# Performance work log

Hardware: AMD Instinct MI355X
Metric: run time of the kernel (lower is better)

## Reference

```python
import jax, jax.numpy as jnp
import numpy as np

# dims: S=seq (attention axis 0), B=batch, Din=input_dim, E=adjusted_dim,
# NEXP=num_experts, HID=expert hidden, DOUT=output_dim, NH=heads, TOPK=top_k
S, B, Din, E, NEXP, HID, DOUT, NH, TOPK = 1024, 8, 768, 768, 10, 256, 768, 8, 2
LN_EPS = 1e-5


def setup_inputs() -> dict:
    key = jax.random.key(0)
    ks = jax.random.split(key, 10)
    s = 0.02
    return {
        "x": jax.random.normal(ks[0], (S, B, Din), jnp.float32),
        # input_projection: Linear(Din -> E)
        "Wp": jax.random.normal(ks[1], (E, Din), jnp.float32) * s,
        "bp": jnp.zeros((E,), jnp.float32),
        # MultiheadAttention packed in-proj (3E, E) and out-proj (E, E)
        "Win": jax.random.normal(ks[2], (3 * E, E), jnp.float32) * s,
        "bin_": jnp.zeros((3 * E,), jnp.float32),
        "Wo": jax.random.normal(ks[3], (E, E), jnp.float32) * s,
        "bo": jnp.zeros((E,), jnp.float32),
        # gate: Linear(E -> NEXP)
        "Wg": jax.random.normal(ks[4], (NEXP, E), jnp.float32) * s,
        "bg": jnp.zeros((NEXP,), jnp.float32),
        # experts: NEXP x (Linear(E->HID), ReLU, Linear(HID->DOUT))
        "W1": jax.random.normal(ks[5], (NEXP, E, HID), jnp.float32) * s,
        "b1": jnp.zeros((NEXP, HID), jnp.float32),
        "W2": jax.random.normal(ks[6], (NEXP, HID, DOUT), jnp.float32) * s,
        "b2": jnp.zeros((NEXP, DOUT), jnp.float32),
        # LayerNorm(DOUT)
        "gamma": jnp.ones((DOUT,), jnp.float32),
        "beta": jnp.zeros((DOUT,), jnp.float32),
    }


def reference(x, Wp, bp, Win, bin_, Wo, bo, Wg, bg, W1, b1, W2, b2, gamma, beta):
    hd = E // NH
    # input projection
    h = jnp.einsum('sbd,ed->sbe', x, Wp) + bp  # (S,B,E)
    # self-attention (torch MHA, seq-first, no mask)
    qkv = jnp.einsum('sbe,fe->sbf', h, Win) + bin_  # (S,B,3E)
    q, k, v = jnp.split(qkv, 3, axis=-1)
    q = q.reshape(S, B, NH, hd) * (hd ** -0.5)
    k = k.reshape(S, B, NH, hd)
    v = v.reshape(S, B, NH, hd)
    scores = jnp.einsum('sbhd,tbhd->bhst', q, k)       # (B,NH,S,S)
    attn = jax.nn.softmax(scores, axis=-1)
    ctx = jnp.einsum('bhst,tbhd->sbhd', attn, v).reshape(S, B, E)
    h = jnp.einsum('sbe,fe->sbf', ctx, Wo) + bo        # (S,B,E)
    # top-k gating
    gate_probs = jax.nn.softmax(jnp.einsum('sbe,ne->sbn', h, Wg) + bg, axis=-1)
    top_p, top_i = jax.lax.top_k(gate_probs, TOPK)     # (S,B,TOPK)
    top_p = top_p / jnp.sum(top_p, axis=-1, keepdims=True)
    # combine weights: (S,B,NEXP), zero for unselected experts
    combine = jnp.sum(top_p[..., None] * jax.nn.one_hot(top_i, NEXP, dtype=h.dtype), axis=-2)
    # per-expert MLP, weighted combine (dense dispatch, same math as masked loop)
    eh = jax.nn.relu(jnp.einsum('sbe,neh->sbnh', h, W1) + b1)  # (S,B,NEXP,HID)
    moe = jnp.einsum('sbnh,nho,sbn->sbo', eh, W2, combine) + jnp.einsum('sbn,no->sbo', combine, b2)
    # LayerNorm over DOUT
    mu = jnp.mean(moe, axis=-1, keepdims=True)
    var = jnp.mean((moe - mu) ** 2, axis=-1, keepdims=True)
    moe = (moe - mu) * jax.lax.rsqrt(var + LN_EPS) * gamma + beta
    # attn_weights: head-averaged (B,S,S), then raw .view to (S,B,-1), mean last
    aw = jnp.mean(attn, axis=1)            # (B,S,S)
    aw = aw.reshape(S, B, -1)              # memory reinterpretation as in torch .view
    aw = jnp.mean(aw, axis=-1, keepdims=True)  # (S,B,1)
    return moe * aw, aw
```

## Files before the change

kernel.cpp:

```cpp
#include <hip/hip_runtime.h>
#include <math.h>

#define S_    1024
#define B_    8
#define E_    768
#define NH_   8
#define HD_   96
#define NEXP_ 10
#define HID_  256
#define DOUT_ 768
#define TOK_  (S_*B_)
#define OUT0_ (TOK_*DOUT_)

#define OFF_H1   0
#define OFF_QB   6291456
#define OFF_KB   12582912
#define OFF_VB   18874368
#define OFF_H2   25165824
#define OFF_TW   31457280
#define OFF_INT  (31457280 + 16384)

__device__ __forceinline__ void gload_lds16(const float* g, float* l) {
    __builtin_amdgcn_global_load_lds((const __attribute__((address_space(1))) void*)(g),
                                     (__attribute__((address_space(3))) void*)(l), 16, 0, 0);
}

__global__ void init_counts(int* counts) {
    if (threadIdx.x < 16) counts[threadIdx.x] = 0;
}

template<int MODE>
__global__ __launch_bounds__(256)
void gemm_abt(const float* __restrict__ A, const float* __restrict__ W,
              const float* __restrict__ bias, float* __restrict__ C,
              int M, int N, int K,
              float* __restrict__ qb, float* __restrict__ kb, float* __restrict__ vb)
{
    __shared__ float Ast[16][132];
    __shared__ float Wst[16][132];
    const int tid = threadIdx.x;
    const int tx = tid & 15, ty = tid >> 4;
    const int m0 = blockIdx.x * 128, n0 = blockIdx.y * 128;
    const int lrow = tid >> 2, lkq = tid & 3;

    const float* Ab0 = A + (size_t)(m0 + lrow)*K + lkq*4;
    const float* Ab1 = Ab0 + (size_t)64*K;
    const float* Wb0 = W + (size_t)(n0 + lrow)*K + lkq*4;
    const float* Wb1 = Wb0 + (size_t)64*K;

    float4 pa0 = *(const float4*)Ab0;
    float4 pa1 = *(const float4*)Ab1;
    float4 pw0 = *(const float4*)Wb0;
    float4 pw1 = *(const float4*)Wb1;

    float acc[8][8];
    #pragma unroll
    for (int i = 0; i < 8; i++)
        #pragma unroll
        for (int j = 0; j < 8; j++) acc[i][j] = 0.f;

    for (int k0 = 0;;) {
        Ast[lkq*4+0][lrow]    = pa0.x; Ast[lkq*4+1][lrow]    = pa0.y;
        Ast[lkq*4+2][lrow]    = pa0.z; Ast[lkq*4+3][lrow]    = pa0.w;
        Ast[lkq*4+0][lrow+64] = pa1.x; Ast[lkq*4+1][lrow+64] = pa1.y;
        Ast[lkq*4+2][lrow+64] = pa1.z; Ast[lkq*4+3][lrow+64] = pa1.w;
        Wst[lkq*4+0][lrow]    = pw0.x; Wst[lkq*4+1][lrow]    = pw0.y;
        Wst[lkq*4+2][lrow]    = pw0.z; Wst[lkq*4+3][lrow]    = pw0.w;
        Wst[lkq*4+0][lrow+64] = pw1.x; Wst[lkq*4+1][lrow+64] = pw1.y;
        Wst[lkq*4+2][lrow+64] = pw1.z; Wst[lkq*4+3][lrow+64] = pw1.w;
        __syncthreads();
        k0 += 16;
        const bool more = (k0 < K);
        if (more) {
            pa0 = *(const float4*)(Ab0 + k0);
            pa1 = *(const float4*)(Ab1 + k0);
            pw0 = *(const float4*)(Wb0 + k0);
            pw1 = *(const float4*)(Wb1 + k0);
        }
        #pragma unroll
        for (int kk = 0; kk < 16; kk++) {
            float a[8], w[8];
            *(float4*)&a[0] = *(const float4*)&Ast[kk][ty*4];
            *(float4*)&a[4] = *(const float4*)&Ast[kk][64 + ty*4];
            *(float4*)&w[0] = *(const float4*)&Wst[kk][tx*4];
            *(float4*)&w[4] = *(const float4*)&Wst[kk][64 + tx*4];
            #pragma unroll
            for (int i = 0; i < 8; i++)
                #pragma unroll
                for (int j = 0; j < 8; j++)
                    acc[i][j] = fmaf(a[i], w[j], acc[i][j]);
        }
        __syncthreads();
        if (!more) break;
    }

    const float QS = 0.10206207261596575f;
    #pragma unroll
    for (int i = 0; i < 8; i++) {
        const int m = m0 + ((i < 4) ? (ty*4 + i) : (64 + ty*4 + i - 4));
        #pragma unroll
        for (int jq = 0; jq < 2; jq++) {
            const int nb = n0 + (jq ? (64 + tx*4) : (tx*4));
            const float4 bv = *(const float4*)(bias + nb);
            float4 v;
            v.x = acc[i][jq*4+0] + bv.x;
            v.y = acc[i][jq*4+1] + bv.y;
            v.z = acc[i][jq*4+2] + bv.z;
            v.w = acc[i][jq*4+3] + bv.w;
            if (MODE == 0) {
                *(float4*)(C + (size_t)m*N + nb) = v;
            } else {
                const int s = m >> 3, b = m & 7;
                const int which = nb / E_;
                const int e = nb - which*E_;
                const int h = e / HD_, d = e - h*HD_;
                float* dst = (which == 0) ? qb : (which == 1) ? kb : vb;
                if (which == 0) { v.x *= QS; v.y *= QS; v.z *= QS; v.w *= QS; }
                *(float4*)(dst + ((size_t)((b<<3) + h)*S_ + s)*HD_ + d) = v;
            }
        }
    }
}

__global__ __launch_bounds__(256, 2)
void attn_kernel(const float* __restrict__ qb, const float* __restrict__ kb,
                 const float* __restrict__ vb, float* __restrict__ ctxb)
{
    __shared__ float Ks[64*96];
    __shared__ float Vs[64*96];
    const int tid = threadIdx.x;
    const int wave = tid >> 6;
    const int lane = tid & 63;
    const int part = lane >> 5;
    const int rloc = wave*32 + (lane & 31);
    const int bh = blockIdx.y;
    const int srow = blockIdx.x*128 + rloc;
    const float* qp = qb + ((size_t)bh*S_ + srow)*HD_;
    const float* kbase = kb + (size_t)bh*S_*HD_;
    const float* vbase = vb + (size_t)bh*S_*HD_;

    float q[96], cx[96];
    #pragma unroll
    for (int i = 0; i < 24; i++) *(float4*)&q[i*4] = *(const float4*)(qp + i*4);
    #pragma unroll
    for (int i = 0; i < 96; i++) cx[i] = 0.f;
    float l = 0.f;

    for (int t0 = 0; t0 < S_; t0 += 64) {
        #pragma unroll
        for (int j = 0; j < 6; j++) {
            const int f = j*256 + tid;
            const int r = f / 24, c = f % 24;
            gload_lds16(kbase + (size_t)(t0+r)*HD_ + c*4, &Ks[f*4]);
            gload_lds16(vbase + (size_t)(t0+r)*HD_ + c*4, &Vs[f*4]);
        }
        __syncthreads();
        const int tb = part*32;
        for (int tt2 = 0; tt2 < 32; tt2++) {
            const float* kr = &Ks[(size_t)(tb+tt2)*96];
            float sacc[4] = {0.f, 0.f, 0.f, 0.f};
            #pragma unroll
            for (int i = 0; i < 24; i++) {
                const float4 kv = *(const float4*)(kr + i*4);
                float sv = sacc[i & 3];
                sv = fmaf(q[i*4+0], kv.x, sv); sv = fmaf(q[i*4+1], kv.y, sv);
                sv = fmaf(q[i*4+2], kv.z, sv); sv = fmaf(q[i*4+3], kv.w, sv);
                sacc[i & 3] = sv;
            }
            const float p = __expf((sacc[0]+sacc[1])+(sacc[2]+sacc[3]));
            l += p;
            const float* vr = &Vs[(size_t)(tb+tt2)*96];
            #pragma unroll
            for (int i = 0; i < 24; i++) {
                const float4 vv = *(const float4*)(vr + i*4);
                cx[i*4+0] = fmaf(p, vv.x, cx[i*4+0]);
                cx[i*4+1] = fmaf(p, vv.y, cx[i*4+1]);
                cx[i*4+2] = fmaf(p, vv.z, cx[i*4+2]);
                cx[i*4+3] = fmaf(p, vv.w, cx[i*4+3]);
            }
        }
        __syncthreads();
    }
    l += __shfl_xor(l, 32);
    #pragma unroll
    for (int i = 0; i < 96; i++) cx[i] += __shfl_xor(cx[i], 32);
    if (part == 0) {
        const float inv = 1.f / l;
        const int b = bh >> 3, h = bh & 7;
        float* op = ctxb + ((size_t)srow*B_ + b)*E_ + h*HD_;
        #pragma unroll
        for (int i = 0; i < 24; i++) {
            float4 o;
            o.x = cx[i*4+0]*inv; o.y = cx[i*4+1]*inv;
            o.z = cx[i*4+2]*inv; o.w = cx[i*4+3]*inv;
            *(float4*)(op + i*4) = o;
        }
    }
}

__global__ __launch_bounds__(256)
void gate_kernel(const float* __restrict__ h2, const float* __restrict__ Wg,
                 const float* __restrict__ bg, int* __restrict__ tix,
                 float* __restrict__ tw, int* __restrict__ counts)
{
    const int lane = threadIdx.x & 63;
    const int tok = blockIdx.x*4 + (threadIdx.x >> 6);
    const float* hr = h2 + (size_t)tok*E_;
    float part[NEXP_];
    #pragma unroll
    for (int n = 0; n < NEXP_; n++) part[n] = 0.f;
    for (int i = 0; i < 12; i++) {
        const float xv = hr[i*64 + lane];
        #pragma unroll
        for (int n = 0; n < NEXP_; n++)
            part[n] = fmaf(xv, Wg[n*E_ + i*64 + lane], part[n]);
    }
    #pragma unroll
    for (int n = 0; n < NEXP_; n++) {
        float v = part[n];
        for (int off = 32; off > 0; off >>= 1) v += __shfl_xor(v, off);
        part[n] = v;
    }
    if (lane == 0) {
        float lg[NEXP_];
        #pragma unroll
        for (int n = 0; n < NEXP_; n++) lg[n] = part[n] + bg[n];
        int i1 = 0; float l1 = lg[0];
        #pragma unroll
        for (int n = 1; n < NEXP_; n++) if (lg[n] > l1) { l1 = lg[n]; i1 = n; }
        int i2 = -1; float l2 = -1e30f;
        #pragma unroll
        for (int n = 0; n < NEXP_; n++) if (n != i1 && lg[n] > l2) { l2 = lg[n]; i2 = n; }
        const float p = __expf(l2 - l1);
        const float w1 = 1.f / (1.f + p);
        tix[tok*2]   = i1; tix[tok*2+1] = i2;
        tw[tok*2]    = w1; tw[tok*2+1]  = 1.f - w1;
        atomicAdd(&counts[i1], 1);
        atomicAdd(&counts[i2], 1);
    }
}

__global__ void scan_kernel(const int* __restrict__ counts, int* __restrict__ offsets,
                            int* __restrict__ cursor) {
    if (threadIdx.x == 0) {
        int run = 0;
        for (int e = 0; e < NEXP_; e++) { offsets[e] = run; cursor[e] = run; run += counts[e]; }
    }
}

__global__ __launch_bounds__(256)
void scatter_kernel(const int* __restrict__ tix, int* __restrict__ cursor,
                    int* __restrict__ elist) {
    const int tok = blockIdx.x*256 + threadIdx.x;
    #pragma unroll
    for (int slot = 0; slot < 2; slot++) {
        const int e = tix[tok*2 + slot];
        const int pos = atomicAdd(&cursor[e], 1);
        elist[pos] = tok*2 + slot;
    }
}

__global__ __launch_bounds__(256)
void expert_mlp1(const float* __restrict__ h2, const float* __restrict__ W1,
                 const float* __restrict__ b1, const int* __restrict__ offsets,
                 const int* __restrict__ counts, const int* __restrict__ elist,
                 float* __restrict__ eh)
{
    const int e = blockIdx.z;
    const int cnt = counts[e];
    const int mt = blockIdx.x;
    if (mt*128 >= cnt) return;
    const int off = offsets[e];
    const int n0 = blockIdx.y * 128;
    __shared__ float Ast[16][132];
    __shared__ float Wst[16][132];
    __shared__ int toks[128];
    const int tid = threadIdx.x;
    const int tx = tid & 15, ty = tid >> 4;
    const int lrow = tid >> 2, lkq = tid & 3;
    if (tid < 128) {
        const int r = mt*128 + tid;
        toks[tid] = (r < cnt) ? (elist[off + r] >> 1) : (elist[off] >> 1);
    }
    __syncthreads();
    const float* W = W1 + (size_t)e*E_*HID_;
    const float* b1e = b1 + (size_t)e*HID_;

    const int kkA = tid >> 5, nqA = tid & 31;
    const int kkB = kkA + 8;
    const float* A0 = h2 + (size_t)toks[lrow]*E_ + lkq*4;
    const float* A1 = h2 + (size_t)toks[lrow+64]*E_ + lkq*4;
    const float* Wq0 = W + (size_t)kkA*HID_ + n0 + nqA*4;
    const float* Wq1 = W + (size_t)kkB*HID_ + n0 + nqA*4;

    float4 pa0 = *(const float4*)A0;
    float4 pa1 = *(const float4*)A1;
    float4 pw0 = *(const float4*)Wq0;
    float4 pw1 = *(const float4*)Wq1;

    float acc[8][8];
    #pragma unroll
    for (int i = 0; i < 8; i++)
        #pragma unroll
        for (int j = 0; j < 8; j++) acc[i][j] = 0.f;

    for (int k0 = 0;;) {
        Ast[lkq*4+0][lrow]    = pa0.x; Ast[lkq*4+1][lrow]    = pa0.y;
        Ast[lkq*4+2][lrow]    = pa0.z; Ast[lkq*4+3][lrow]    = pa0.w;
        Ast[lkq*4+0][lrow+64] = pa1.x; Ast[lkq*4+1][lrow+64] = pa1.y;
        Ast[lkq*4+2][lrow+64] = pa1.z; Ast[lkq*4+3][lrow+64] = pa1.w;
        *(float4*)&Wst[kkA][nqA*4] = pw0;
        *(float4*)&Wst[kkB][nqA*4] = pw1;
        __syncthreads();
        k0 += 16;
        const bool more = (k0 < E_);
        if (more) {
            pa0 = *(const float4*)(A0 + k0);
            pa1 = *(const float4*)(A1 + k0);
            pw0 = *(const float4*)(Wq0 + (size_t)k0*HID_);
            pw1 = *(const float4*)(Wq1 + (size_t)k0*HID_);
        }
        #pragma unroll
        for (int kk = 0; kk < 16; kk++) {
            float a[8], w[8];
            *(float4*)&a[0] = *(const float4*)&Ast[kk][ty*4];
            *(float4*)&a[4] = *(const float4*)&Ast[kk][64 + ty*4];
            *(float4*)&w[0] = *(const float4*)&Wst[kk][tx*4];
            *(float4*)&w[4] = *(const float4*)&Wst[kk][64 + tx*4];
            #pragma unroll
            for (int i = 0; i < 8; i++)
                #pragma unroll
                for (int j = 0; j < 8; j++)
                    acc[i][j] = fmaf(a[i], w[j], acc[i][j]);
        }
        __syncthreads();
        if (!more) break;
    }
    #pragma unroll
    for (int i = 0; i < 8; i++) {
        const int ri = (i < 4) ? (ty*4 + i) : (64 + ty*4 + i - 4);
        const int r = mt*128 + ri;
        if (r >= cnt) continue;
        const size_t pos = (size_t)(off + r);
        #pragma unroll
        for (int jq = 0; jq < 2; jq++) {
            const int nb = n0 + (jq ? (64 + tx*4) : (tx*4));
            const float4 bv = *(const float4*)(b1e + nb);
            float4 v;
            v.x = fmaxf(acc[i][jq*4+0] + bv.x, 0.f);
            v.y = fmaxf(acc[i][jq*4+1] + bv.y, 0.f);
            v.z = fmaxf(acc[i][jq*4+2] + bv.z, 0.f);
            v.w = fmaxf(acc[i][jq*4+3] + bv.w, 0.f);
            *(float4*)(eh + pos*HID_ + nb) = v;
        }
    }
}

__global__ __launch_bounds__(256)
void expert_mlp2(const float* __restrict__ eh, const float* __restrict__ W2,
                 const float* __restrict__ b2, const float* __restrict__ tw,
                 const int* __restrict__ offsets, const int* __restrict__ counts,
                 const int* __restrict__ elist,
                 float* __restrict__ moe0, float* __restrict__ moe1)
{
    const int e = blockIdx.z;
    const int cnt = counts[e];
    const int mt = blockIdx.x;
    if (mt*128 >= cnt) return;
    const int off = offsets[e];
    const int n0 = blockIdx.y * 128;
    __shared__ float Ast[16][132];
    __shared__ float Wst[16][132];
    __shared__ int ents[128];
    __shared__ float tws[128];
    const int tid = threadIdx.x;
    const int tx = tid & 15, ty = tid >> 4;
    const int lrow = tid >> 2, lkq = tid & 3;
    if (tid < 128) {
        const int r = mt*128 + tid;
        const int ent = (r < cnt) ? elist[off + r] : elist[off];
        ents[tid] = ent;
        tws[tid] = tw[ent];
    }
    __syncthreads();
    const float* W = W2 + (size_t)e*HID_*DOUT_;
    const float* b2e = b2 + (size_t)e*DOUT_;

    const int kkA = tid >> 5, nqA = tid & 31;
    const int kkB = kkA + 8;
    const size_t posA = (size_t)(off + ((mt*128 + lrow      < cnt) ? (mt*128 + lrow)      : 0));
    const size_t posB = (size_t)(off + ((mt*128 + lrow + 64 < cnt) ? (mt*128 + lrow + 64) : 0));
    const float* A0 = eh + posA*HID_ + lkq*4;
    const float* A1 = eh + posB*HID_ + lkq*4;
    const float* Wq0 = W + (size_t)kkA*DOUT_ + n0 + nqA*4;
    const float* Wq1 = W + (size_t)kkB*DOUT_ + n0 + nqA*4;

    float4 pa0 = *(const float4*)A0;
    float4 pa1 = *(const float4*)A1;
    float4 pw0 = *(const float4*)Wq0;
    float4 pw1 = *(const float4*)Wq1;

    float acc[8][8];
    #pragma unroll
    for (int i = 0; i < 8; i++)
        #pragma unroll
        for (int j = 0; j < 8; j++) acc[i][j] = 0.f;

    for (int k0 = 0;;) {
        Ast[lkq*4+0][lrow]    = pa0.x; Ast[lkq*4+1][lrow]    = pa0.y;
        Ast[lkq*4+2][lrow]    = pa0.z; Ast[lkq*4+3][lrow]    = pa0.w;
        Ast[lkq*4+0][lrow+64] = pa1.x; Ast[lkq*4+1][lrow+64] = pa1.y;
        Ast[lkq*4+2][lrow+64] = pa1.z; Ast[lkq*4+3][lrow+64] = pa1.w;
        *(float4*)&Wst[kkA][nqA*4] = pw0;
        *(float4*)&Wst[kkB][nqA*4] = pw1;
        __syncthreads();
        k0 += 16;
        const bool more = (k0 < HID_);
        if (more) {
            pa0 = *(const float4*)(A0 + k0);
            pa1 = *(const float4*)(A1 + k0);
            pw0 = *(const float4*)(Wq0 + (size_t)k0*DOUT_);
            pw1 = *(const float4*)(Wq1 + (size_t)k0*DOUT_);
        }
        #pragma unroll
        for (int kk = 0; kk < 16; kk++) {
            float a[8], w[8];
            *(float4*)&a[0] = *(const float4*)&Ast[kk][ty*4];
            *(float4*)&a[4] = *(const float4*)&Ast[kk][64 + ty*4];
            *(float4*)&w[0] = *(const float4*)&Wst[kk][tx*4];
            *(float4*)&w[4] = *(const float4*)&Wst[kk][64 + tx*4];
            #pragma unroll
            for (int i = 0; i < 8; i++)
                #pragma unroll
                for (int j = 0; j < 8; j++)
                    acc[i][j] = fmaf(a[i], w[j], acc[i][j]);
        }
        __syncthreads();
        if (!more) break;
    }
    #pragma unroll
    for (int i = 0; i < 8; i++) {
        const int ri = (i < 4) ? (ty*4 + i) : (64 + ty*4 + i - 4);
        const int r = mt*128 + ri;
        if (r >= cnt) continue;
        const int ent = ents[ri];
        const int tok = ent >> 1;
        const float wt = tws[ri];
        float* dst = (ent & 1) ? moe1 : moe0;
        #pragma unroll
        for (int jq = 0; jq < 2; jq++) {
            const int nb = n0 + (jq ? (64 + tx*4) : (tx*4));
            const float4 bv = *(const float4*)(b2e + nb);
            float4 v;
            v.x = (acc[i][jq*4+0] + bv.x) * wt;
            v.y = (acc[i][jq*4+1] + bv.y) * wt;
            v.z = (acc[i][jq*4+2] + bv.z) * wt;
            v.w = (acc[i][jq*4+3] + bv.w) * wt;
            *(float4*)(dst + (size_t)tok*DOUT_ + nb) = v;
        }
    }
}

__global__ __launch_bounds__(256)
void ln_kernel(const float* __restrict__ m0b, const float* __restrict__ m1b,
               const float* __restrict__ gamma, const float* __restrict__ beta,
               float* __restrict__ out)
{
    __shared__ float red[8];
    const int tk = blockIdx.x;
    const int tid = threadIdx.x;
    float v[3];
    float s = 0.f;
    #pragma unroll
    for (int j = 0; j < 3; j++) {
        const int c = tid + j*256;
        v[j] = m0b[(size_t)tk*DOUT_ + c] + m1b[(size_t)tk*DOUT_ + c];
        s += v[j];
    }
    for (int off = 32; off > 0; off >>= 1) s += __shfl_xor(s, off);
    if ((tid & 63) == 0) red[tid >> 6] = s;
    __syncthreads();
    const float mu = (red[0]+red[1]+red[2]+red[3]) * (1.f/768.f);
    float s2 = 0.f;
    #pragma unroll
    for (int j = 0; j < 3; j++) { const float d = v[j] - mu; s2 += d*d; }
    for (int off = 32; off > 0; off >>= 1) s2 += __shfl_xor(s2, off);
    if ((tid & 63) == 0) red[4 + (tid >> 6)] = s2;
    __syncthreads();
    const float var = (red[4]+red[5]+red[6]+red[7]) * (1.f/768.f);
    const float rs = rsqrtf(var + 1e-5f);
    const float AW = 0.0009765625f;
    #pragma unroll
    for (int j = 0; j < 3; j++) {
        const int c = tid + j*256;
        out[(size_t)tk*DOUT_ + c] = ((v[j] - mu)*rs*gamma[c] + beta[c]) * AW;
    }
    if (tid == 0) out[OUT0_ + tk] = AW;
}

extern "C" void kernel_launch(void* const* d_in, const int* in_sizes, int n_in,
                              void* d_out, int out_size, void* d_ws, size_t ws_size,
                              hipStream_t stream)
{
    const float* x    = (const float*)d_in[0];
    const float* Wp   = (const float*)d_in[1];
    const float* bp   = (const float*)d_in[2];
    const float* Win  = (const float*)d_in[3];
    const float* binp = (const float*)d_in[4];
    const float* Wo   = (const float*)d_in[5];
    const float* bo   = (const float*)d_in[6];
    const float* Wg   = (const float*)d_in[7];
    const float* bg   = (const float*)d_in[8];
    const float* W1   = (const float*)d_in[9];
    const float* b1   = (const float*)d_in[10];
    const float* W2   = (const float*)d_in[11];
    const float* b2   = (const float*)d_in[12];
    const float* gamma= (const float*)d_in[13];
    const float* beta = (const float*)d_in[14];
    float* out = (float*)d_out;

    float* wsf  = (float*)d_ws;
    float* h1   = wsf + OFF_H1;
    float* qb   = wsf + OFF_QB;
    float* kb   = wsf + OFF_KB;
    float* vb   = wsf + OFF_VB;
    float* h2   = wsf + OFF_H2;
    float* ctx  = h1;
    float* eh   = qb;
    float* moe0 = kb;
    float* moe1 = vb;
    float* tw   = wsf + OFF_TW;
    int* ib     = (int*)(wsf + OFF_INT);
    int* tix    = ib;
    int* elist  = ib + 16384;
    int* counts = ib + 32768;
    int* offs   = ib + 32768 + 16;
    int* cursor = ib + 32768 + 32;

    init_counts<<<1, 64, 0, stream>>>(counts);
    gemm_abt<0><<<dim3(64, 6), 256, 0, stream>>>(x, Wp, bp, h1, TOK_, E_, E_, nullptr, nullptr, nullptr);
    gemm_abt<1><<<dim3(64, 18), 256, 0, stream>>>(h1, Win, binp, nullptr, TOK_, 3*E_, E_, qb, kb, vb);
    attn_kernel<<<dim3(8, 64), 256, 0, stream>>>(qb, kb, vb, ctx);
    gemm_abt<0><<<dim3(64, 6), 256, 0, stream>>>(ctx, Wo, bo, h2, TOK_, E_, E_, nullptr, nullptr, nullptr);
    gate_kernel<<<2048, 256, 0, stream>>>(h2, Wg, bg, tix, tw, counts);
    scan_kernel<<<1, 64, 0, stream>>>(counts, offs, cursor);
    scatter_kernel<<<32, 256, 0, stream>>>(tix, cursor, elist);
    expert_mlp1<<<dim3(64, 2, NEXP_), 256, 0, stream>>>(h2, W1, b1, offs, counts, elist, eh);
    expert_mlp2<<<dim3(64, 6, NEXP_), 256, 0, stream>>>(eh, W2, b2, tw, offs, counts, elist, moe0, moe1);
    ln_kernel<<<TOK_, 256, 0, stream>>>(moe0, moe1, gamma, beta, out);
    (void)in_sizes; (void)n_in; (void)out_size; (void)ws_size;
}
```

Before: 2.211 ms.

## Shrink GEMM N-tile to 64 and split attention head dim across lane pairs

The dense GEMMs now use 128x64 tiles with an 8x4 per-thread accumulator, which doubles the grid and cuts registers per thread. The attention kernel splits each query row's 96-wide head dimension across two lanes, which combine partial scores with a shuffle. It also splits the key range across two more lanes and uses 32-row K/V tiles, raising the occupancy hint from 2 to 4 blocks. The aim is more resident waves and less register pressure, at the cost of extra shuffles, lower per-thread reuse in the GEMM, and more LDS syncs per key.

Measured after the change: 2.433 ms. 1.1x slower.

```diff
diff --git a/kernel.cpp b/kernel.cpp
--- a/kernel.cpp
+++ b/kernel.cpp
@@ -31,33 +31,31 @@
 
 template<int MODE>
 __global__ __launch_bounds__(256)
-void gemm_abt(const float* __restrict__ A, const float* __restrict__ W,
-              const float* __restrict__ bias, float* __restrict__ C,
-              int M, int N, int K,
-              float* __restrict__ qb, float* __restrict__ kb, float* __restrict__ vb)
+void gemm64(const float* __restrict__ A, const float* __restrict__ W,
+            const float* __restrict__ bias, float* __restrict__ C,
+            int M, int N, int K,
+            float* __restrict__ qb, float* __restrict__ kb, float* __restrict__ vb)
 {
     __shared__ float Ast[16][132];
-    __shared__ float Wst[16][132];
+    __shared__ float Wst[16][68];
     const int tid = threadIdx.x;
     const int tx = tid & 15, ty = tid >> 4;
-    const int m0 = blockIdx.x * 128, n0 = blockIdx.y * 128;
+    const int m0 = blockIdx.x * 128, n0 = blockIdx.y * 64;
     const int lrow = tid >> 2, lkq = tid & 3;
 
     const float* Ab0 = A + (size_t)(m0 + lrow)*K + lkq*4;
     const float* Ab1 = Ab0 + (size_t)64*K;
     const float* Wb0 = W + (size_t)(n0 + lrow)*K + lkq*4;
-    const float* Wb1 = Wb0 + (size_t)64*K;
 
     float4 pa0 = *(const float4*)Ab0;
     float4 pa1 = *(const float4*)Ab1;
     float4 pw0 = *(const float4*)Wb0;
-    float4 pw1 = *(const float4*)Wb1;
-
-    float acc[8][8];
+
+    float acc[8][4];
     #pragma unroll
     for (int i = 0; i < 8; i++)
         #pragma unroll
-        for (int j = 0; j < 8; j++) acc[i][j] = 0.f;
+        for (int j = 0; j < 4; j++) acc[i][j] = 0.f;
 
     for (int k0 = 0;;) {
         Ast[lkq*4+0][lrow]    = pa0.x; Ast[lkq*4+1][lrow]    = pa0.y;
@@ -66,8 +64,6 @@
         Ast[lkq*4+2][lrow+64] = pa1.z; Ast[lkq*4+3][lrow+64] = pa1.w;
         Wst[lkq*4+0][lrow]    = pw0.x; Wst[lkq*4+1][lrow]    = pw0.y;
         Wst[lkq*4+2][lrow]    = pw0.z; Wst[lkq*4+3][lrow]    = pw0.w;
-        Wst[lkq*4+0][lrow+64] = pw1.x; Wst[lkq*4+1][lrow+64] = pw1.y;
-        Wst[lkq*4+2][lrow+64] = pw1.z; Wst[lkq*4+3][lrow+64] = pw1.w;
         __syncthreads();
         k0 += 16;
         const bool more = (k0 < K);
@@ -75,19 +71,17 @@
             pa0 = *(const float4*)(Ab0 + k0);
             pa1 = *(const float4*)(Ab1 + k0);
             pw0 = *(const float4*)(Wb0 + k0);
-            pw1 = *(const float4*)(Wb1 + k0);
         }
         #pragma unroll
         for (int kk = 0; kk < 16; kk++) {
-            float a[8], w[8];
+            float a[8], w[4];
             *(float4*)&a[0] = *(const float4*)&Ast[kk][ty*4];
             *(float4*)&a[4] = *(const float4*)&Ast[kk][64 + ty*4];
             *(float4*)&w[0] = *(const float4*)&Wst[kk][tx*4];
-            *(float4*)&w[4] = *(const float4*)&Wst[kk][64 + tx*4];
             #pragma unroll
             for (int i = 0; i < 8; i++)
                 #pragma unroll
-                for (int j = 0; j < 8; j++)
+                for (int j = 0; j < 4; j++)
                     acc[i][j] = fmaf(a[i], w[j], acc[i][j]);
         }
         __syncthreads();
@@ -95,83 +89,84 @@
     }
 
     const float QS = 0.10206207261596575f;
+    const int nb = n0 + tx*4;
+    const float4 bv = *(const float4*)(bias + nb);
     #pragma unroll
     for (int i = 0; i < 8; i++) {
         const int m = m0 + ((i < 4) ? (ty*4 + i) : (64 + ty*4 + i - 4));
-        #pragma unroll
-        for (int jq = 0; jq < 2; jq++) {
-            const int nb = n0 + (jq ? (64 + tx*4) : (tx*4));
-            const float4 bv = *(const float4*)(bias + nb);
-            float4 v;
-            v.x = acc[i][jq*4+0] + bv.x;
-            v.y = acc[i][jq*4+1] + bv.y;
-            v.z = acc[i][jq*4+2] + bv.z;
-            v.w = acc[i][jq*4+3] + bv.w;
-            if (MODE == 0) {
-                *(float4*)(C + (size_t)m*N + nb) = v;
-            } else {
-                const int s = m >> 3, b = m & 7;
-                const int which = nb / E_;
-                const int e = nb - which*E_;
-                const int h = e / HD_, d = e - h*HD_;
-                float* dst = (which == 0) ? qb : (which == 1) ? kb : vb;
-                if (which == 0) { v.x *= QS; v.y *= QS; v.z *= QS; v.w *= QS; }
-                *(float4*)(dst + ((size_t)((b<<3) + h)*S_ + s)*HD_ + d) = v;
-            }
-        }
-    }
-}
-
-__global__ __launch_bounds__(256, 2)
+        float4 v;
+        v.x = acc[i][0] + bv.x;
+        v.y = acc[i][1] + bv.y;
+        v.z = acc[i][2] + bv.z;
+        v.w = acc[i][3] + bv.w;
+        if (MODE == 0) {
+            *(float4*)(C + (size_t)m*N + nb) = v;
+        } else {
+            const int s = m >> 3, b = m & 7;
+            const int which = nb / E_;
+            const int e = nb - which*E_;
+            const int h = e / HD_, d = e - h*HD_;
+            float* dst = (which == 0) ? qb : (which == 1) ? kb : vb;
+            if (which == 0) { v.x *= QS; v.y *= QS; v.z *= QS; v.w *= QS; }
+            *(float4*)(dst + ((size_t)((b<<3) + h)*S_ + s)*HD_ + d) = v;
+        }
+    }
+}
+
+__global__ __launch_bounds__(256, 4)
 void attn_kernel(const float* __restrict__ qb, const float* __restrict__ kb,
                  const float* __restrict__ vb, float* __restrict__ ctxb)
 {
-    __shared__ float Ks[64*96];
-    __shared__ float Vs[64*96];
+    __shared__ float Ks[32*96];
+    __shared__ float Vs[32*96];
     const int tid = threadIdx.x;
     const int wave = tid >> 6;
     const int lane = tid & 63;
-    const int part = lane >> 5;
-    const int rloc = wave*32 + (lane & 31);
+    const int p_d = lane & 1;
+    const int p_t = (lane >> 1) & 1;
+    const int rloc = wave*16 + (lane >> 2);
     const int bh = blockIdx.y;
-    const int srow = blockIdx.x*128 + rloc;
-    const float* qp = qb + ((size_t)bh*S_ + srow)*HD_;
+    const int srow = blockIdx.x*64 + rloc;
+    const float* qp = qb + ((size_t)bh*S_ + srow)*HD_ + p_d*48;
     const float* kbase = kb + (size_t)bh*S_*HD_;
     const float* vbase = vb + (size_t)bh*S_*HD_;
 
-    float q[96], cx[96];
-    #pragma unroll
-    for (int i = 0; i < 24; i++) *(float4*)&q[i*4] = *(const float4*)(qp + i*4);
-    #pragma unroll
-    for (int i = 0; i < 96; i++) cx[i] = 0.f;
+    float q[48], cx[48];
+    #pragma unroll
+    for (int i = 0; i < 12; i++) *(float4*)&q[i*4] = *(const float4*)(qp + i*4);
+    #pragma unroll
+    for (int i = 0; i < 48; i++) cx[i] = 0.f;
     float l = 0.f;
 
-    for (int t0 = 0; t0 < S_; t0 += 64) {
-        #pragma unroll
-        for (int j = 0; j < 6; j++) {
+    for (int t0 = 0; t0 < S_; t0 += 32) {
+        #pragma unroll
+        for (int j = 0; j < 3; j++) {
             const int f = j*256 + tid;
             const int r = f / 24, c = f % 24;
             gload_lds16(kbase + (size_t)(t0+r)*HD_ + c*4, &Ks[f*4]);
             gload_lds16(vbase + (size_t)(t0+r)*HD_ + c*4, &Vs[f*4]);
         }
         __syncthreads();
-        const int tb = part*32;
-        for (int tt2 = 0; tt2 < 32; tt2++) {
-            const float* kr = &Ks[(size_t)(tb+tt2)*96];
+        const int tb = p_t*16;
+        #pragma unroll 2
+        for (int k = 0; k < 16; k++) {
+            const float* kr = &Ks[(tb+k)*96 + p_d*48];
             float sacc[4] = {0.f, 0.f, 0.f, 0.f};
             #pragma unroll
-            for (int i = 0; i < 24; i++) {
+            for (int i = 0; i < 12; i++) {
                 const float4 kv = *(const float4*)(kr + i*4);
                 float sv = sacc[i & 3];
                 sv = fmaf(q[i*4+0], kv.x, sv); sv = fmaf(q[i*4+1], kv.y, sv);
                 sv = fmaf(q[i*4+2], kv.z, sv); sv = fmaf(q[i*4+3], kv.w, sv);
                 sacc[i & 3] = sv;
             }
-            const float p = __expf((sacc[0]+sacc[1])+(sacc[2]+sacc[3]));
+            float sp = (sacc[0]+sacc[1])+(sacc[2]+sacc[3]);
+            sp += __shfl_xor(sp, 1);
+            const float p = __expf(sp);
             l += p;
-            const float* vr = &Vs[(size_t)(tb+tt2)*96];
+            const float* vr = &Vs[(tb+k)*96 + p_d*48];
             #pragma unroll
-            for (int i = 0; i < 24; i++) {
+            for (int i = 0; i < 12; i++) {
                 const float4 vv = *(const float4*)(vr + i*4);
                 cx[i*4+0] = fmaf(p, vv.x, cx[i*4+0]);
                 cx[i*4+1] = fmaf(p, vv.y, cx[i*4+1]);
@@ -181,15 +176,15 @@
         }
         __syncthreads();
     }
-    l += __shfl_xor(l, 32);
-    #pragma unroll
-    for (int i = 0; i < 96; i++) cx[i] += __shfl_xor(cx[i], 32);
-    if (part == 0) {
+    l += __shfl_xor(l, 2);
+    #pragma unroll
+    for (int i = 0; i < 48; i++) cx[i] += __shfl_xor(cx[i], 2);
+    if (p_t == 0) {
         const float inv = 1.f / l;
         const int b = bh >> 3, h = bh & 7;
-        float* op = ctxb + ((size_t)srow*B_ + b)*E_ + h*HD_;
-        #pragma unroll
-        for (int i = 0; i < 24; i++) {
+        float* op = ctxb + ((size_t)srow*B_ + b)*E_ + h*HD_ + p_d*48;
+        #pragma unroll
+        for (int i = 0; i < 12; i++) {
             float4 o;
             o.x = cx[i*4+0]*inv; o.y = cx[i*4+1]*inv;
             o.z = cx[i*4+2]*inv; o.w = cx[i*4+3]*inv;
@@ -538,10 +533,10 @@
     int* cursor = ib + 32768 + 32;
 
     init_counts<<<1, 64, 0, stream>>>(counts);
-    gemm_abt<0><<<dim3(64, 6), 256, 0, stream>>>(x, Wp, bp, h1, TOK_, E_, E_, nullptr, nullptr, nullptr);
-    gemm_abt<1><<<dim3(64, 18), 256, 0, stream>>>(h1, Win, binp, nullptr, TOK_, 3*E_, E_, qb, kb, vb);
-    attn_kernel<<<dim3(8, 64), 256, 0, stream>>>(qb, kb, vb, ctx);
-    gemm_abt<0><<<dim3(64, 6), 256, 0, stream>>>(ctx, Wo, bo, h2, TOK_, E_, E_, nullptr, nullptr, nullptr);
+    gemm64<0><<<dim3(64, 12), 256, 0, stream>>>(x, Wp, bp, h1, TOK_, E_, E_, nullptr, nullptr, nullptr);
+    gemm64<1><<<dim3(64, 36), 256, 0, stream>>>(h1, Win, binp, nullptr, TOK_, 3*E_, E_, qb, kb, vb);
+    attn_kernel<<<dim3(16, 64), 256, 0, stream>>>(qb, kb, vb, ctx);
+    gemm64<0><<<dim3(64, 12), 256, 0, stream>>>(ctx, Wo, bo, h2, TOK_, E_, E_, nullptr, nullptr, nullptr);
     gate_kernel<<<2048, 256, 0, stream>>>(h2, Wg, bg, tix, tw, counts);
     scan_kernel<<<1, 64, 0, stream>>>(counts, offs, cursor);
     scatter_kernel<<<32, 256, 0, stream>>>(tix, cursor, elist);
```
